# Optimization experiments

Measured on AMD Instinct MI355X. Metric: run time of the kernel, lower is better.

The kernel has to match this reference:

```python
import jax, jax.numpy as jnp
import numpy as np
import math

N_NODES = 100_000
N_EDGES = 800_000
NODE_DIM = 128
EDGE_DIM = 64
HIDDEN = 128
HEADS = 8
HEAD_DIM = HIDDEN // HEADS


def _segment_softmax(scores, seg, n):
    # scores: [E, H], grouped by destination node `seg`
    m = jax.ops.segment_max(scores, seg, num_segments=n)
    e = jnp.exp(scores - m[seg])
    d = jax.ops.segment_sum(e, seg, num_segments=n)
    return e / d[seg]


def _layer_norm(x, g, b, eps=1e-5):
    mu = jnp.mean(x, axis=-1, keepdims=True)
    var = jnp.mean((x - mu) ** 2, axis=-1, keepdims=True)
    return (x - mu) * jax.lax.rsqrt(var + eps) * g + b


def _graph_conv(x, row, col, edge_proj, Wn, b, n):
    # PyG GraphConvolution: add self-loops, symmetric deg normalization,
    # msg = (Wn x)[row] + edge_lin(edge_attr); aggregate (add) at col.
    # Self-loop edges carry zero edge features (edge_lin has no bias -> contributes 0).
    loop = jnp.arange(n)
    row2 = jnp.concatenate([row, loop])
    col2 = jnp.concatenate([col, loop])
    ep2 = jnp.concatenate([edge_proj, jnp.zeros((n, edge_proj.shape[1]), edge_proj.dtype)])
    deg = jax.ops.segment_sum(jnp.ones_like(col2, x.dtype), col2, num_segments=n)
    dinv = jnp.where(deg > 0, jax.lax.rsqrt(jnp.maximum(deg, 1e-12)), 0.0)
    norm = dinv[row2] * dinv[col2]
    h = x @ Wn                                   # [n, hidden]
    msg = (h[row2] + ep2) * norm[:, None]        # [E+n, hidden]
    return jax.ops.segment_sum(msg, col2, num_segments=n) + b


def setup_inputs() -> dict:
    key = jax.random.key(0)
    ks = jax.random.split(key, 20)

    def xav(k, shape):
        fan_in, fan_out = shape[0], shape[-1]
        s = math.sqrt(2.0 / (fan_in + fan_out))
        return jax.random.normal(k, shape, jnp.float32) * s

    return {
        "x": jax.random.normal(ks[0], (N_NODES, NODE_DIM), jnp.float32),
        "edge_index": jax.random.randint(ks[1], (2, N_EDGES), 0, N_NODES, jnp.int64),
        "edge_attr": jax.random.normal(ks[2], (N_EDGES, EDGE_DIM), jnp.float32),
        "W_qkv": xav(ks[3], (NODE_DIM, 3 * HIDDEN)),
        "b_qkv": jnp.zeros((3 * HIDDEN,), jnp.float32),
        "W_ek": xav(ks[4], (EDGE_DIM, HIDDEN)),
        "b_ek": jnp.zeros((HIDDEN,), jnp.float32),
        "W_n1": xav(ks[5], (NODE_DIM, HIDDEN)),
        "W_e1": xav(ks[6], (EDGE_DIM, HIDDEN)),
        "b1": jnp.zeros((HIDDEN,), jnp.float32),
        "W_n2": xav(ks[7], (HIDDEN, HIDDEN)),
        "W_e2": xav(ks[8], (EDGE_DIM, HIDDEN)),
        "b2": jnp.zeros((HIDDEN,), jnp.float32),
        "W_out": xav(ks[9], (HIDDEN, NODE_DIM)),
        "b_out": jnp.zeros((NODE_DIM,), jnp.float32),
        "ln_g": jnp.ones((NODE_DIM,), jnp.float32),
        "ln_b": jnp.zeros((NODE_DIM,), jnp.float32),
    }


def reference(x, edge_index, edge_attr, W_qkv, b_qkv, W_ek, b_ek,
              W_n1, W_e1, b1, W_n2, W_e2, b2, W_out, b_out, ln_g, ln_b):
    n = x.shape[0]
    row, col = edge_index[0], edge_index[1]

    # --- compute_dynamic_edges (computed in the original forward but its
    # result is discarded; kept here for fidelity to the source math) ---
    qkv = x @ W_qkv + b_qkv
    q, k, _v = jnp.split(qkv, 3, axis=-1)
    q = q.reshape(n, HEADS, HEAD_DIM)
    k = k.reshape(n, HEADS, HEAD_DIM)
    ek = (edge_attr @ W_ek + b_ek).reshape(-1, HEADS, HEAD_DIM)
    scores = jnp.sum(q[row] * (k[col] + ek), axis=-1) / math.sqrt(HEAD_DIM)  # [E, H]
    _edge_weights = _segment_softmax(scores, col, n)  # unused downstream (as in source)

    # --- two GraphConvolution layers (dropout is identity in eval mode) ---
    h1 = jax.nn.gelu(_graph_conv(x, row, col, edge_attr @ W_e1, W_n1, b1, n), approximate=False)
    h2 = jax.nn.gelu(_graph_conv(h1, row, col, edge_attr @ W_e2, W_n2, b2, n), approximate=False)

    out = h2 @ W_out + b_out
    return _layer_norm(out + x, ln_g, ln_b)
```

## Files before the change

### kernel.cpp

```cpp
#include <hip/hip_runtime.h>
#include <math.h>

#define N_NODES 100000
#define N_EDGES 800000
#define NBLK 391

__device__ __forceinline__ float gelu_f(float v) {
    return 0.5f * v * (1.0f + erff(v * 0.70710678f));
}

__global__ void k_count(const int* __restrict__ col, int* __restrict__ cnt) {
    int e = blockIdx.x * 256 + threadIdx.x;
    if (e < N_EDGES) {
        unsigned c = (unsigned)col[e];
        if (c < N_NODES) atomicAdd(&cnt[c], 1);
    }
}

__global__ void k_blocksum(const int* __restrict__ cnt, int* __restrict__ bsum) {
    __shared__ int sc[256];
    int t = threadIdx.x, i = blockIdx.x * 256 + t;
    sc[t] = (i < N_NODES) ? cnt[i] : 0;
    __syncthreads();
    for (int o = 128; o; o >>= 1) {
        if (t < o) sc[t] += sc[t + o];
        __syncthreads();
    }
    if (t == 0) bsum[blockIdx.x] = sc[0];
}

__global__ void k_scanblocks(const int* __restrict__ bsum, int* __restrict__ bexcl) {
    __shared__ int s[512];
    int t = threadIdx.x;
    s[t] = (t < NBLK) ? bsum[t] : 0;
    __syncthreads();
    for (int o = 1; o < 512; o <<= 1) {
        int v = (t >= o) ? s[t - o] : 0;
        __syncthreads();
        s[t] += v;
        __syncthreads();
    }
    if (t < NBLK) bexcl[t] = t ? s[t - 1] : 0;
}

__global__ void k_offsets(const int* __restrict__ cnt, const int* __restrict__ bexcl,
                          int* __restrict__ off, int* __restrict__ pos,
                          int2* __restrict__ offcnt, float* __restrict__ dinv) {
    __shared__ int sc[256];
    int t = threadIdx.x, i = blockIdx.x * 256 + t;
    int v = (i < N_NODES) ? cnt[i] : 0;
    sc[t] = v;
    __syncthreads();
    for (int o = 1; o < 256; o <<= 1) {
        int tv = (t >= o) ? sc[t - o] : 0;
        __syncthreads();
        sc[t] += tv;
        __syncthreads();
    }
    if (i < N_NODES) {
        int s = bexcl[blockIdx.x] + (sc[t] - v);
        off[i] = s;
        pos[i] = s;
        if (offcnt) offcnt[i] = make_int2(s, v);
        dinv[i] = rsqrtf((float)(v + 1));
    }
}

__global__ void k_build(const int* __restrict__ row, const int* __restrict__ col,
                        int* __restrict__ pos, const float* __restrict__ dinv,
                        int4* __restrict__ edge) {
    int e = blockIdx.x * 256 + threadIdx.x;
    if (e < N_EDGES) {
        unsigned r = (unsigned)row[e], c = (unsigned)col[e];
        if (r < N_NODES && c < N_NODES) {
            int slot = atomicAdd(&pos[c], 1);
            edge[slot] = make_int4((int)r, e, __float_as_int(dinv[r]), 0);
        }
    }
}

template<int MODE>
__global__ __launch_bounds__(256) void k_gather(
    const float* __restrict__ X, const float* __restrict__ EAraw,
    const int2* __restrict__ offcnt, const int4* __restrict__ edge,
    const float* __restrict__ dinv, float* __restrict__ act)
{
    int w = threadIdx.x >> 6, l = threadIdx.x & 63;
    int c = blockIdx.x * 4 + w;
    if (c >= N_NODES) return;
    int2 oc = offcnt[c];
    int beg = __builtin_amdgcn_readfirstlane(oc.x);
    int d   = __builtin_amdgcn_readfirstlane(oc.y);
    const float2* X2 = (const float2*)X;

    float2 xc = X2[(size_t)c * 64 + l];
    float dv = dinv[c];

    int sU[16]; float vU[16]; int eU[16];
    #pragma unroll
    for (int i = 0; i < 16; i++) {
        int4 E = edge[beg + i];
        sU[i] = E.x;
        eU[i] = E.y;
        vU[i] = __int_as_float(E.z);
    }
    int s0 = (d > 0) ? sU[0] : 0;
    int e0 = (d > 0) ? eU[0] : 0;
    #pragma unroll
    for (int i = 0; i < 16; i++) {
        if (i >= d) {
            vU[i] = 0.f;
            sU[i] = s0;
            eU[i] = e0;
        }
    }

    float2 xv[16];
    #pragma unroll
    for (int i = 0; i < 16; i++) xv[i] = X2[(size_t)sU[i] * 64 + l];
    float evv[16];
    if (MODE == 0) {
        #pragma unroll
        for (int i = 0; i < 16; i++) evv[i] = EAraw[(size_t)eU[i] * 64 + l];
    }

    float a0 = 0.f, a1 = 0.f, ae = 0.f;
    #pragma unroll
    for (int i = 0; i < 16; i++) {
        a0 += vU[i] * xv[i].x;
        a1 += vU[i] * xv[i].y;
        if (MODE == 0) ae += vU[i] * evv[i];
    }

    for (int j = 16; j < d; j++) {
        int4 E = edge[beg + j];
        float v = __int_as_float(E.z);
        float2 x = X2[(size_t)E.x * 64 + l];
        a0 += v * x.x;
        a1 += v * x.y;
        if (MODE == 0) ae += v * EAraw[(size_t)E.y * 64 + l];
    }

    float dv2 = dv * dv;
    float* arow = act + (size_t)c * 192;
    ((float2*)arow)[l] = make_float2(dv * a0 + dv2 * xc.x, dv * a1 + dv2 * xc.y);
    if (MODE == 0) arow[128 + l] = dv * ae;
}

__global__ __launch_bounds__(128, 3) void k_gemm(
    const float* __restrict__ act,
    const float* __restrict__ Wn, const float* __restrict__ We,
    const float* __restrict__ bias, float* __restrict__ out)
{
    __shared__ float sact[32][192];
    int t = threadIdx.x;
    int w = t >> 6, l = t & 63;
    int h = l >> 5, q = l & 31;

    size_t base = (size_t)blockIdx.x * (32 * 192);
    #pragma unroll
    for (int i = 0; i < 12; i++) {
        *(float4*)&sact[0][(i * 128 + t) * 4] =
            *(const float4*)(act + base + (size_t)(i * 128 + t) * 4);
    }
    __syncthreads();

    int rbase = w * 16 + h * 8;
    int row0  = blockIdx.x * 32 + rbase;
    float4 acc[8] = {};

    const float4* Wn4 = (const float4*)Wn;
    const float4* We4 = (const float4*)We;

    float4 n0 = Wn4[q], n1 = Wn4[32 + q], n2 = Wn4[64 + q], n3 = Wn4[96 + q];
    for (int k = 0; k < 192; k += 4) {
        float4 w0 = n0, w1 = n1, w2 = n2, w3 = n3;
        int kn = k + 4;
        if (kn < 192) {
            const float4* Wp = (kn < 128) ? (Wn4 + (size_t)kn * 32)
                                          : (We4 + (size_t)(kn - 128) * 32);
            n0 = Wp[q]; n1 = Wp[32 + q]; n2 = Wp[64 + q]; n3 = Wp[96 + q];
        }
        #pragma unroll
        for (int r = 0; r < 8; r++) {
            float4 a = *(const float4*)&sact[rbase + r][k];
            acc[r].x += a.x * w0.x + a.y * w1.x + a.z * w2.x + a.w * w3.x;
            acc[r].y += a.x * w0.y + a.y * w1.y + a.z * w2.y + a.w * w3.y;
            acc[r].z += a.x * w0.z + a.y * w1.z + a.z * w2.z + a.w * w3.z;
            acc[r].w += a.x * w0.w + a.y * w1.w + a.z * w2.w + a.w * w3.w;
        }
    }

    float4 bb = ((const float4*)bias)[q];
    #pragma unroll
    for (int r = 0; r < 8; r++) {
        float4 v;
        v.x = gelu_f(acc[r].x + bb.x);
        v.y = gelu_f(acc[r].y + bb.y);
        v.z = gelu_f(acc[r].z + bb.z);
        v.w = gelu_f(acc[r].w + bb.w);
        ((float4*)out)[(size_t)(row0 + r) * 32 + q] = v;
    }
}

__global__ __launch_bounds__(128, 3) void k_gemm_final(
    const float* __restrict__ act,
    const float* __restrict__ Wn, const float* __restrict__ We,
    const float* __restrict__ bias, const float* __restrict__ x,
    const float* __restrict__ Wo, const float* __restrict__ bo,
    const float* __restrict__ g, const float* __restrict__ lb,
    float* __restrict__ out)
{
    __shared__ float sact[32][192];
    int t = threadIdx.x;
    int w = t >> 6, l = t & 63;
    int h = l >> 5, q = l & 31;

    size_t base = (size_t)blockIdx.x * (32 * 192);
    #pragma unroll
    for (int i = 0; i < 12; i++) {
        *(float4*)&sact[0][(i * 128 + t) * 4] =
            *(const float4*)(act + base + (size_t)(i * 128 + t) * 4);
    }
    __syncthreads();

    int rbase = w * 16 + h * 8;
    int row0  = blockIdx.x * 32 + rbase;
    float4 acc[8] = {};

    const float4* Wn4 = (const float4*)Wn;
    const float4* We4 = (const float4*)We;
    const float4* Wo4 = (const float4*)Wo;

    float4 n0 = Wn4[q], n1 = Wn4[32 + q], n2 = Wn4[64 + q], n3 = Wn4[96 + q];
    for (int k = 0; k < 192; k += 4) {
        float4 w0 = n0, w1 = n1, w2 = n2, w3 = n3;
        int kn = k + 4;
        const float4* Wp = (kn < 128) ? (Wn4 + (size_t)kn * 32)
                         : (kn < 192) ? (We4 + (size_t)(kn - 128) * 32)
                                      : Wo4;
        n0 = Wp[q]; n1 = Wp[32 + q]; n2 = Wp[64 + q]; n3 = Wp[96 + q];
        #pragma unroll
        for (int r = 0; r < 8; r++) {
            float4 a = *(const float4*)&sact[rbase + r][k];
            acc[r].x += a.x * w0.x + a.y * w1.x + a.z * w2.x + a.w * w3.x;
            acc[r].y += a.x * w0.y + a.y * w1.y + a.z * w2.y + a.w * w3.y;
            acc[r].z += a.x * w0.z + a.y * w1.z + a.z * w2.z + a.w * w3.z;
            acc[r].w += a.x * w0.w + a.y * w1.w + a.z * w2.w + a.w * w3.w;
        }
    }

    float4 bb = ((const float4*)bias)[q];
    #pragma unroll
    for (int r = 0; r < 8; r++) {
        float4 v;
        v.x = gelu_f(acc[r].x + bb.x);
        v.y = gelu_f(acc[r].y + bb.y);
        v.z = gelu_f(acc[r].z + bb.z);
        v.w = gelu_f(acc[r].w + bb.w);
        *(float4*)&sact[rbase + r][4 * q] = v;
        acc[r] = make_float4(0.f, 0.f, 0.f, 0.f);
    }

    for (int k = 0; k < 128; k += 4) {
        float4 w0 = n0, w1 = n1, w2 = n2, w3 = n3;
        int kn = k + 4;
        if (kn < 128) {
            const float4* Wp = Wo4 + (size_t)kn * 32;
            n0 = Wp[q]; n1 = Wp[32 + q]; n2 = Wp[64 + q]; n3 = Wp[96 + q];
        }
        #pragma unroll
        for (int r = 0; r < 8; r++) {
            float4 a = *(const float4*)&sact[rbase + r][k];
            acc[r].x += a.x * w0.x + a.y * w1.x + a.z * w2.x + a.w * w3.x;
            acc[r].y += a.x * w0.y + a.y * w1.y + a.z * w2.y + a.w * w3.y;
            acc[r].z += a.x * w0.z + a.y * w1.z + a.z * w2.z + a.w * w3.z;
            acc[r].w += a.x * w0.w + a.y * w1.w + a.z * w2.w + a.w * w3.w;
        }
    }

    float4 bov = ((const float4*)bo)[q];
    float4 gv  = ((const float4*)g)[q];
    float4 lbv = ((const float4*)lb)[q];
    const float4* X4 = (const float4*)x;

    #pragma unroll
    for (int r = 0; r < 8; r++) {
        int c = row0 + r;
        float4 xv = X4[(size_t)c * 32 + q];
        float v0 = acc[r].x + bov.x + xv.x;
        float v1 = acc[r].y + bov.y + xv.y;
        float v2 = acc[r].z + bov.z + xv.z;
        float v3 = acc[r].w + bov.w + xv.w;
        float s = (v0 + v1) + (v2 + v3);
        #pragma unroll
        for (int o = 16; o; o >>= 1) s += __shfl_xor(s, o, 64);
        float mu = s * (1.0f / 128.0f);
        float d0 = v0 - mu, d1 = v1 - mu, d2 = v2 - mu, d3 = v3 - mu;
        float sq = (d0 * d0 + d1 * d1) + (d2 * d2 + d3 * d3);
        #pragma unroll
        for (int o = 16; o; o >>= 1) sq += __shfl_xor(sq, o, 64);
        float rs = rsqrtf(sq * (1.0f / 128.0f) + 1e-5f);
        float4 ov;
        ov.x = d0 * rs * gv.x + lbv.x;
        ov.y = d1 * rs * gv.y + lbv.y;
        ov.z = d2 * rs * gv.z + lbv.z;
        ov.w = d3 * rs * gv.w + lbv.w;
        ((float4*)out)[(size_t)c * 32 + q] = ov;
    }
}

__global__ __launch_bounds__(256) void k_layer(
    const float* __restrict__ X, const float* __restrict__ EAraw,
    const float* __restrict__ EaIn, float* __restrict__ EaOut,
    const int* __restrict__ off, const int* __restrict__ cnt,
    const int4* __restrict__ edge, const float* __restrict__ dinv,
    const float* __restrict__ Wn, const float* __restrict__ We,
    const float* __restrict__ bias, float* __restrict__ out, int mode)
{
    __shared__ float act[4][4][192];
    int w = threadIdx.x >> 6, l = threadIdx.x & 63;
    int row0 = blockIdx.x * 16 + w * 4;

    for (int r = 0; r < 4; r++) {
        int c = row0 + r;
        int beg = off[c];
        int d = cnt[c];
        float a0 = 0.f, a1 = 0.f, ae = 0.f;
        for (int j = 0; j < d; j++) {
            int4 E = edge[beg + j];
            unsigned s = (unsigned)E.x;
            if (s >= N_NODES) continue;
            float sv = __int_as_float(E.z);
            float2 xv = ((const float2*)X)[s * 64 + l];
            a0 += sv * xv.x;
            a1 += sv * xv.y;
            if (mode == 0) {
                unsigned e = (unsigned)E.y;
                if (e < N_EDGES) ae += sv * EAraw[e * 64 + l];
            }
        }
        float dv = dinv[c], dv2 = dv * dv;
        float2 xc = ((const float2*)X)[c * 64 + l];
        act[w][r][2 * l]     = dv * a0 + dv2 * xc.x;
        act[w][r][2 * l + 1] = dv * a1 + dv2 * xc.y;
        if (mode == 0) {
            act[w][r][128 + l] = dv * ae;
            EaOut[c * 64 + l] = ae;
        } else {
            act[w][r][128 + l] = dv * EaIn[c * 64 + l];
        }
    }
    __syncthreads();

    float acc[4][2] = {};
    for (int k = 0; k < 128; k++) {
        float2 wv = ((const float2*)Wn)[k * 64 + l];
        #pragma unroll
        for (int r = 0; r < 4; r++) {
            float a = act[w][r][k];
            acc[r][0] += a * wv.x;
            acc[r][1] += a * wv.y;
        }
    }
    for (int k = 0; k < 64; k++) {
        float2 wv = ((const float2*)We)[k * 64 + l];
        #pragma unroll
        for (int r = 0; r < 4; r++) {
            float a = act[w][r][128 + k];
            acc[r][0] += a * wv.x;
            acc[r][1] += a * wv.y;
        }
    }

    float2 bb = ((const float2*)bias)[l];
    for (int r = 0; r < 4; r++) {
        float v0 = acc[r][0] + bb.x;
        float v1 = acc[r][1] + bb.y;
        ((float2*)out)[(row0 + r) * 64 + l] = make_float2(gelu_f(v0), gelu_f(v1));
    }
}

__global__ __launch_bounds__(256) void k_final(
    const float* __restrict__ h2, const float* __restrict__ x,
    const float* __restrict__ Wo, const float* __restrict__ bo,
    const float* __restrict__ g, const float* __restrict__ lb,
    float* __restrict__ out)
{
    __shared__ float lds[4][4][128];
    int w = threadIdx.x >> 6, l = threadIdx.x & 63;
    int row0 = blockIdx.x * 16 + w * 4;

    for (int r = 0; r < 4; r++) {
        int c = row0 + r;
        float2 hv = ((const float2*)h2)[(size_t)c * 64 + l];
        lds[w][r][2 * l]     = hv.x;
        lds[w][r][2 * l + 1] = hv.y;
    }
    __syncthreads();

    float acc[4][2] = {};
    const float2* Wo2 = (const float2*)Wo;
    for (int k = 0; k < 128; k += 4) {
        float2 w0 = Wo2[(k + 0) * 64 + l];
        float2 w1 = Wo2[(k + 1) * 64 + l];
        float2 w2 = Wo2[(k + 2) * 64 + l];
        float2 w3 = Wo2[(k + 3) * 64 + l];
        #pragma unroll
        for (int r = 0; r < 4; r++) {
            float4 a = *(const float4*)&lds[w][r][k];
            acc[r][0] += a.x * w0.x + a.y * w1.x + a.z * w2.x + a.w * w3.x;
            acc[r][1] += a.x * w0.y + a.y * w1.y + a.z * w2.y + a.w * w3.y;
        }
    }

    float2 bov = ((const float2*)bo)[l];
    float2 gv  = ((const float2*)g)[l];
    float2 lbv = ((const float2*)lb)[l];

    for (int r = 0; r < 4; r++) {
        int c = row0 + r;
        float2 xv = ((const float2*)x)[(size_t)c * 64 + l];
        float v0 = acc[r][0] + bov.x + xv.x;
        float v1 = acc[r][1] + bov.y + xv.y;
        float s = v0 + v1;
        #pragma unroll
        for (int o = 32; o; o >>= 1) s += __shfl_xor(s, o, 64);
        float mu = s * (1.0f / 128.0f);
        float d0 = v0 - mu, d1 = v1 - mu;
        float sq = d0 * d0 + d1 * d1;
        #pragma unroll
        for (int o = 32; o; o >>= 1) sq += __shfl_xor(sq, o, 64);
        float rs = rsqrtf(sq * (1.0f / 128.0f) + 1e-5f);
        float2 ov;
        ov.x = d0 * rs * gv.x + lbv.x;
        ov.y = d1 * rs * gv.y + lbv.y;
        ((float2*)out)[(size_t)c * 64 + l] = ov;
    }
}

extern "C" void kernel_launch(void* const* d_in, const int* in_sizes, int n_in,
                              void* d_out, int out_size, void* d_ws, size_t ws_size,
                              hipStream_t stream)
{
    const float* x   = (const float*)d_in[0];
    const int*   ei  = (const int*)d_in[1];
    const float* ea  = (const float*)d_in[2];
    const float* Wn1 = (const float*)d_in[7];
    const float* We1 = (const float*)d_in[8];
    const float* b1  = (const float*)d_in[9];
    const float* Wn2 = (const float*)d_in[10];
    const float* We2 = (const float*)d_in[11];
    const float* b2  = (const float*)d_in[12];
    const float* Wo  = (const float*)d_in[13];
    const float* bo  = (const float*)d_in[14];
    const float* lng = (const float*)d_in[15];
    const float* lnb = (const float*)d_in[16];
    const int* row = ei;
    const int* col = ei + N_EDGES;

    char* ws = (char*)d_ws;
    size_t off_b = 0;
    auto alloc = [&](size_t bytes) {
        void* p = ws + off_b;
        off_b += (bytes + 255) & ~(size_t)255;
        return p;
    };
    int*   cnt   = (int*)  alloc((size_t)N_NODES * 4);
    int*   off   = (int*)  alloc((size_t)N_NODES * 4);
    int*   pos   = (int*)  alloc((size_t)N_NODES * 4);
    int*   bsum  = (int*)  alloc((size_t)NBLK * 4);
    int*   bexcl = (int*)  alloc((size_t)NBLK * 4);
    float* dinv  = (float*)alloc((size_t)N_NODES * 4);
    int4*  edge  = (int4*) alloc((size_t)(N_EDGES + 16) * 16);
    float* h1    = (float*)alloc((size_t)N_NODES * 128 * 4);
    size_t common_end = off_b;

    int2*  offcnt = (int2*) alloc((size_t)N_NODES * 8);
    float* act    = (float*)alloc((size_t)N_NODES * 192 * 4);
    size_t split_end = off_b;

    float* Ea = (float*)(ws + common_end);
    size_t fused_end = common_end + (((size_t)N_NODES * 64 * 4 + 255) & ~(size_t)255);

    bool use_split = (split_end <= ws_size);
    if (!use_split && fused_end > ws_size) return;

    float* h2 = (float*)d_out;

    hipMemsetAsync(cnt, 0, (size_t)N_NODES * 4, stream);

    k_count     <<<(N_EDGES + 255) / 256, 256, 0, stream>>>(col, cnt);
    k_blocksum  <<<NBLK, 256, 0, stream>>>(cnt, bsum);
    k_scanblocks<<<1, 512, 0, stream>>>(bsum, bexcl);
    k_offsets   <<<NBLK, 256, 0, stream>>>(cnt, bexcl, off, pos,
                                           use_split ? offcnt : nullptr, dinv);
    k_build     <<<(N_EDGES + 255) / 256, 256, 0, stream>>>(row, col, pos, dinv, edge);

    if (use_split) {
        k_gather<0><<<(N_NODES + 3) / 4, 256, 0, stream>>>(x, ea, offcnt,
                                                           edge, dinv, act);
        k_gemm     <<<N_NODES / 32, 128, 0, stream>>>(act, Wn1, We1, b1, h1);
        k_gather<1><<<(N_NODES + 3) / 4, 256, 0, stream>>>(h1, nullptr, offcnt,
                                                           edge, dinv, act);
        k_gemm_final<<<N_NODES / 32, 128, 0, stream>>>(
            act, Wn2, We2, b2, x, Wo, bo, lng, lnb, (float*)d_out);
    } else {
        k_layer<<<N_NODES / 16, 256, 0, stream>>>(x, ea, nullptr, Ea,
                                                  off, cnt, edge, dinv,
                                                  Wn1, We1, b1, h1, 0);
        k_layer<<<N_NODES / 16, 256, 0, stream>>>(h1, nullptr, Ea, nullptr,
                                                  off, cnt, edge, dinv,
                                                  Wn2, We2, b2, h2, 1);
        k_final<<<N_NODES / 16, 256, 0, stream>>>(h2, x, Wo, bo, lng, lnb, (float*)d_out);
    }
}
```

Before: 806.2 us.

## Fuse neighbor gather into GEMM kernels via shared memory staging

Merges each gather kernel with its following dense GEMM kernel, so aggregated rows are written straight into shared memory instead of a 192-wide global activation buffer. The per-node edge-attribute aggregate is computed once in layer 1, stored in a 64-wide buffer, and reused by layer 2 instead of being recomputed. The fused kernel uses 256 threads per 32 rows with 4 rows per thread rather than 8. Each wave now gathers 8 nodes one after another, which may expose gather latency and lowers the memory-level parallelism available per block.

```diff
diff --git a/kernel.cpp b/kernel.cpp
--- a/kernel.cpp
+++ b/kernel.cpp
@@ -80,153 +80,93 @@
 }
 
 template<int MODE>
-__global__ __launch_bounds__(256) void k_gather(
+__global__ __launch_bounds__(256, 2) void k_fused(
     const float* __restrict__ X, const float* __restrict__ EAraw,
     const int2* __restrict__ offcnt, const int4* __restrict__ edge,
-    const float* __restrict__ dinv, float* __restrict__ act)
-{
-    int w = threadIdx.x >> 6, l = threadIdx.x & 63;
-    int c = blockIdx.x * 4 + w;
-    if (c >= N_NODES) return;
-    int2 oc = offcnt[c];
-    int beg = __builtin_amdgcn_readfirstlane(oc.x);
-    int d   = __builtin_amdgcn_readfirstlane(oc.y);
-    const float2* X2 = (const float2*)X;
-
-    float2 xc = X2[(size_t)c * 64 + l];
-    float dv = dinv[c];
-
-    int sU[16]; float vU[16]; int eU[16];
-    #pragma unroll
-    for (int i = 0; i < 16; i++) {
-        int4 E = edge[beg + i];
-        sU[i] = E.x;
-        eU[i] = E.y;
-        vU[i] = __int_as_float(E.z);
-    }
-    int s0 = (d > 0) ? sU[0] : 0;
-    int e0 = (d > 0) ? eU[0] : 0;
-    #pragma unroll
-    for (int i = 0; i < 16; i++) {
-        if (i >= d) {
-            vU[i] = 0.f;
-            sU[i] = s0;
-            eU[i] = e0;
-        }
-    }
-
-    float2 xv[16];
-    #pragma unroll
-    for (int i = 0; i < 16; i++) xv[i] = X2[(size_t)sU[i] * 64 + l];
-    float evv[16];
-    if (MODE == 0) {
-        #pragma unroll
-        for (int i = 0; i < 16; i++) evv[i] = EAraw[(size_t)eU[i] * 64 + l];
-    }
-
-    float a0 = 0.f, a1 = 0.f, ae = 0.f;
-    #pragma unroll
-    for (int i = 0; i < 16; i++) {
-        a0 += vU[i] * xv[i].x;
-        a1 += vU[i] * xv[i].y;
-        if (MODE == 0) ae += vU[i] * evv[i];
-    }
-
-    for (int j = 16; j < d; j++) {
-        int4 E = edge[beg + j];
-        float v = __int_as_float(E.z);
-        float2 x = X2[(size_t)E.x * 64 + l];
-        a0 += v * x.x;
-        a1 += v * x.y;
-        if (MODE == 0) ae += v * EAraw[(size_t)E.y * 64 + l];
-    }
-
-    float dv2 = dv * dv;
-    float* arow = act + (size_t)c * 192;
-    ((float2*)arow)[l] = make_float2(dv * a0 + dv2 * xc.x, dv * a1 + dv2 * xc.y);
-    if (MODE == 0) arow[128 + l] = dv * ae;
-}
-
-__global__ __launch_bounds__(128, 3) void k_gemm(
-    const float* __restrict__ act,
+    const float* __restrict__ dinv, float* __restrict__ EaS,
     const float* __restrict__ Wn, const float* __restrict__ We,
-    const float* __restrict__ bias, float* __restrict__ out)
-{
-    __shared__ float sact[32][192];
-    int t = threadIdx.x;
-    int w = t >> 6, l = t & 63;
-    int h = l >> 5, q = l & 31;
-
-    size_t base = (size_t)blockIdx.x * (32 * 192);
-    #pragma unroll
-    for (int i = 0; i < 12; i++) {
-        *(float4*)&sact[0][(i * 128 + t) * 4] =
-            *(const float4*)(act + base + (size_t)(i * 128 + t) * 4);
-    }
-    __syncthreads();
-
-    int rbase = w * 16 + h * 8;
-    int row0  = blockIdx.x * 32 + rbase;
-    float4 acc[8] = {};
-
-    const float4* Wn4 = (const float4*)Wn;
-    const float4* We4 = (const float4*)We;
-
-    float4 n0 = Wn4[q], n1 = Wn4[32 + q], n2 = Wn4[64 + q], n3 = Wn4[96 + q];
-    for (int k = 0; k < 192; k += 4) {
-        float4 w0 = n0, w1 = n1, w2 = n2, w3 = n3;
-        int kn = k + 4;
-        if (kn < 192) {
-            const float4* Wp = (kn < 128) ? (Wn4 + (size_t)kn * 32)
-                                          : (We4 + (size_t)(kn - 128) * 32);
-            n0 = Wp[q]; n1 = Wp[32 + q]; n2 = Wp[64 + q]; n3 = Wp[96 + q];
-        }
-        #pragma unroll
-        for (int r = 0; r < 8; r++) {
-            float4 a = *(const float4*)&sact[rbase + r][k];
-            acc[r].x += a.x * w0.x + a.y * w1.x + a.z * w2.x + a.w * w3.x;
-            acc[r].y += a.x * w0.y + a.y * w1.y + a.z * w2.y + a.w * w3.y;
-            acc[r].z += a.x * w0.z + a.y * w1.z + a.z * w2.z + a.w * w3.z;
-            acc[r].w += a.x * w0.w + a.y * w1.w + a.z * w2.w + a.w * w3.w;
-        }
-    }
-
-    float4 bb = ((const float4*)bias)[q];
-    #pragma unroll
-    for (int r = 0; r < 8; r++) {
-        float4 v;
-        v.x = gelu_f(acc[r].x + bb.x);
-        v.y = gelu_f(acc[r].y + bb.y);
-        v.z = gelu_f(acc[r].z + bb.z);
-        v.w = gelu_f(acc[r].w + bb.w);
-        ((float4*)out)[(size_t)(row0 + r) * 32 + q] = v;
-    }
-}
-
-__global__ __launch_bounds__(128, 3) void k_gemm_final(
-    const float* __restrict__ act,
-    const float* __restrict__ Wn, const float* __restrict__ We,
-    const float* __restrict__ bias, const float* __restrict__ x,
-    const float* __restrict__ Wo, const float* __restrict__ bo,
-    const float* __restrict__ g, const float* __restrict__ lb,
+    const float* __restrict__ bias,
+    const float* __restrict__ xres, const float* __restrict__ Wo,
+    const float* __restrict__ bo, const float* __restrict__ g,
+    const float* __restrict__ lb,
     float* __restrict__ out)
 {
     __shared__ float sact[32][192];
     int t = threadIdx.x;
     int w = t >> 6, l = t & 63;
+
+    const float2* X2 = (const float2*)X;
+    for (int j = 0; j < 8; j++) {
+        int c = blockIdx.x * 32 + w * 8 + j;
+        int2 oc = offcnt[c];
+        int beg = __builtin_amdgcn_readfirstlane(oc.x);
+        int d   = __builtin_amdgcn_readfirstlane(oc.y);
+
+        float2 xc = X2[(size_t)c * 64 + l];
+        float dv = dinv[c];
+
+        int sU[16]; float vU[16]; int eU[16];
+        #pragma unroll
+        for (int i = 0; i < 16; i++) {
+            int4 E = edge[beg + i];
+            sU[i] = E.x;
+            eU[i] = E.y;
+            vU[i] = __int_as_float(E.z);
+        }
+        int s0 = (d > 0) ? sU[0] : 0;
+        int e0 = (d > 0) ? eU[0] : 0;
+        #pragma unroll
+        for (int i = 0; i < 16; i++) {
+            if (i >= d) {
+                vU[i] = 0.f;
+                sU[i] = s0;
+                eU[i] = e0;
+            }
+        }
+
+        float2 xv[16];
+        #pragma unroll
+        for (int i = 0; i < 16; i++) xv[i] = X2[(size_t)sU[i] * 64 + l];
+        float evv[16];
+        if (MODE == 0) {
+            #pragma unroll
+            for (int i = 0; i < 16; i++) evv[i] = EAraw[(size_t)eU[i] * 64 + l];
+        }
+
+        float a0 = 0.f, a1 = 0.f, ae = 0.f;
+        #pragma unroll
+        for (int i = 0; i < 16; i++) {
+            a0 += vU[i] * xv[i].x;
+            a1 += vU[i] * xv[i].y;
+            if (MODE == 0) ae += vU[i] * evv[i];
+        }
+        for (int jj = 16; jj < d; jj++) {
+            int4 E = edge[beg + jj];
+            float v = __int_as_float(E.z);
+            float2 xx = X2[(size_t)E.x * 64 + l];
+            a0 += v * xx.x;
+            a1 += v * xx.y;
+            if (MODE == 0) ae += v * EAraw[(size_t)E.y * 64 + l];
+        }
+
+        float dv2 = dv * dv;
+        int rr = w * 8 + j;
+        sact[rr][2 * l]     = dv * a0 + dv2 * xc.x;
+        sact[rr][2 * l + 1] = dv * a1 + dv2 * xc.y;
+        if (MODE == 0) {
+            float s = dv * ae;
+            sact[rr][128 + l] = s;
+            EaS[(size_t)c * 64 + l] = s;
+        } else {
+            sact[rr][128 + l] = EaS[(size_t)c * 64 + l];
+        }
+    }
+    __syncthreads();
+
     int h = l >> 5, q = l & 31;
-
-    size_t base = (size_t)blockIdx.x * (32 * 192);
-    #pragma unroll
-    for (int i = 0; i < 12; i++) {
-        *(float4*)&sact[0][(i * 128 + t) * 4] =
-            *(const float4*)(act + base + (size_t)(i * 128 + t) * 4);
-    }
-    __syncthreads();
-
-    int rbase = w * 16 + h * 8;
+    int rbase = w * 8 + h * 4;
     int row0  = blockIdx.x * 32 + rbase;
-    float4 acc[8] = {};
+    float4 acc[4] = {};
 
     const float4* Wn4 = (const float4*)Wn;
     const float4* We4 = (const float4*)We;
@@ -238,10 +178,10 @@
         int kn = k + 4;
         const float4* Wp = (kn < 128) ? (Wn4 + (size_t)kn * 32)
                          : (kn < 192) ? (We4 + (size_t)(kn - 128) * 32)
-                                      : Wo4;
+                         : (MODE == 1 ? Wo4 : Wn4);
         n0 = Wp[q]; n1 = Wp[32 + q]; n2 = Wp[64 + q]; n3 = Wp[96 + q];
         #pragma unroll
-        for (int r = 0; r < 8; r++) {
+        for (int r = 0; r < 4; r++) {
             float4 a = *(const float4*)&sact[rbase + r][k];
             acc[r].x += a.x * w0.x + a.y * w1.x + a.z * w2.x + a.w * w3.x;
             acc[r].y += a.x * w0.y + a.y * w1.y + a.z * w2.y + a.w * w3.y;
@@ -251,8 +191,22 @@
     }
 
     float4 bb = ((const float4*)bias)[q];
+
+    if (MODE == 0) {
+        #pragma unroll
+        for (int r = 0; r < 4; r++) {
+            float4 v;
+            v.x = gelu_f(acc[r].x + bb.x);
+            v.y = gelu_f(acc[r].y + bb.y);
+            v.z = gelu_f(acc[r].z + bb.z);
+            v.w = gelu_f(acc[r].w + bb.w);
+            ((float4*)out)[(size_t)(row0 + r) * 32 + q] = v;
+        }
+        return;
+    }
+
     #pragma unroll
-    for (int r = 0; r < 8; r++) {
+    for (int r = 0; r < 4; r++) {
         float4 v;
         v.x = gelu_f(acc[r].x + bb.x);
         v.y = gelu_f(acc[r].y + bb.y);
@@ -270,7 +224,7 @@
             n0 = Wp[q]; n1 = Wp[32 + q]; n2 = Wp[64 + q]; n3 = Wp[96 + q];
         }
         #pragma unroll
-        for (int r = 0; r < 8; r++) {
+        for (int r = 0; r < 4; r++) {
             float4 a = *(const float4*)&sact[rbase + r][k];
             acc[r].x += a.x * w0.x + a.y * w1.x + a.z * w2.x + a.w * w3.x;
             acc[r].y += a.x * w0.y + a.y * w1.y + a.z * w2.y + a.w * w3.y;
@@ -282,10 +236,10 @@
     float4 bov = ((const float4*)bo)[q];
     float4 gv  = ((const float4*)g)[q];
     float4 lbv = ((const float4*)lb)[q];
-    const float4* X4 = (const float4*)x;
+    const float4* X4 = (const float4*)xres;
 
     #pragma unroll
-    for (int r = 0; r < 8; r++) {
+    for (int r = 0; r < 4; r++) {
         int c = row0 + r;
         float4 xv = X4[(size_t)c * 32 + q];
         float v0 = acc[r].x + bov.x + xv.x;
@@ -477,7 +431,7 @@
     size_t common_end = off_b;
 
     int2*  offcnt = (int2*) alloc((size_t)N_NODES * 8);
-    float* act    = (float*)alloc((size_t)N_NODES * 192 * 4);
+    float* EaS    = (float*)alloc((size_t)N_NODES * 64 * 4);
     size_t split_end = off_b;
 
     float* Ea = (float*)(ws + common_end);
@@ -498,13 +452,12 @@
     k_build     <<<(N_EDGES + 255) / 256, 256, 0, stream>>>(row, col, pos, dinv, edge);
 
     if (use_split) {
-        k_gather<0><<<(N_NODES + 3) / 4, 256, 0, stream>>>(x, ea, offcnt,
-                                                           edge, dinv, act);
-        k_gemm     <<<N_NODES / 32, 128, 0, stream>>>(act, Wn1, We1, b1, h1);
-        k_gather<1><<<(N_NODES + 3) / 4, 256, 0, stream>>>(h1, nullptr, offcnt,
-                                                           edge, dinv, act);
-        k_gemm_final<<<N_NODES / 32, 128, 0, stream>>>(
-            act, Wn2, We2, b2, x, Wo, bo, lng, lnb, (float*)d_out);
+        k_fused<0><<<N_NODES / 32, 256, 0, stream>>>(
+            x, ea, offcnt, edge, dinv, EaS,
+            Wn1, We1, b1, nullptr, nullptr, nullptr, nullptr, nullptr, h1);
+        k_fused<1><<<N_NODES / 32, 256, 0, stream>>>(
+            h1, nullptr, offcnt, edge, dinv, EaS,
+            Wn2, We2, b2, x, Wo, bo, lng, lnb, (float*)d_out);
     } else {
         k_layer<<<N_NODES / 16, 256, 0, stream>>>(x, ea, nullptr, Ea,
                                                   off, cnt, edge, dinv,
```

New measurement: 805.3 us. About the same (-0.1%).
